# Kernel optimization log

Measured on AMD Instinct MI355X. Metric: run time of the kernel, lower is better.

The kernel has to match this reference:

```python
import jax, jax.numpy as jnp
import numpy as np

B, S, D, H, HD, KVH, FF = 2, 2048, 2048, 16, 128, 1, 8192
EPS = 1e-6
ROPE_BASE = 10000.0
NEG = -1e9


def _rms_norm(x, w):
    return x * jax.lax.rsqrt(jnp.mean(x * x, axis=-1, keepdims=True) + EPS) * w


def _rope(t):
    # t: [B, S, H, HD]; standard rotate-half RoPE
    half = HD // 2
    inv_freq = ROPE_BASE ** (-jnp.arange(0, HD, 2, dtype=jnp.float32) / HD)  # [half]
    ang = jnp.arange(S, dtype=jnp.float32)[:, None] * inv_freq               # [S, half]
    cos = jnp.concatenate([jnp.cos(ang), jnp.cos(ang)], axis=-1)[None, :, None, :]
    sin = jnp.concatenate([jnp.sin(ang), jnp.sin(ang)], axis=-1)[None, :, None, :]
    t1, t2 = t[..., :half], t[..., half:]
    rot = jnp.concatenate([-t2, t1], axis=-1)
    return t * cos + rot * sin


def _alibi_bias():
    # slopes for power-of-two head count: 2^(-8*(h+1)/H)
    slopes = 2.0 ** (-8.0 * (jnp.arange(H, dtype=jnp.float32) + 1.0) / H)    # [H]
    pos = jnp.arange(S, dtype=jnp.float32)
    dist = jnp.abs(pos[:, None] - pos[None, :])                              # [S, S]
    return (-slopes[:, None, None] * dist)[None]                             # [1, H, S, S]


def setup_inputs() -> dict:
    key = jax.random.key(0)
    ks = jax.random.split(key, 8)
    sc = lambda fan: 1.0 / np.sqrt(fan)
    x = jax.random.normal(ks[0], (B, S, D), jnp.float32)
    causal = jnp.where(jnp.tril(jnp.ones((S, S), bool)), 0.0, NEG).astype(jnp.float32)[None, None]
    return {
        "x": x,
        "mask": causal,                                                       # [1,1,S,S]
        "w_norm1": jnp.ones((D,), jnp.float32),
        "w_norm2": jnp.ones((D,), jnp.float32),
        "q_w": jax.random.normal(ks[1], (D, D), jnp.float32) * sc(D),        # [out,in] torch layout
        "kv_w": jax.random.normal(ks[2], (KVH * HD * 2, D), jnp.float32) * sc(D),
        "o_w": jax.random.normal(ks[3], (D, D), jnp.float32) * sc(D),
        "w1": jax.random.normal(ks[4], (FF, D), jnp.float32) * sc(D),
        "w2": jax.random.normal(ks[5], (FF, D), jnp.float32) * sc(D),
        "w3": jax.random.normal(ks[6], (D, FF), jnp.float32) * sc(FF),
    }


def reference(x, mask, w_norm1, w_norm2, q_w, kv_w, o_w, w1, w2, w3):
    # --- attention sub-block (pre-norm) ---
    h = _rms_norm(x, w_norm1)
    q = (h @ q_w.T).reshape(B, S, H, HD)                                      # [B,S,H,HD]
    kv = (h @ kv_w.T).reshape(B, S, KVH, 2, HD)
    k = jnp.broadcast_to(kv[:, :, :, 0, :], (B, S, H, HD))                    # MQA expand
    v = jnp.broadcast_to(kv[:, :, :, 1, :], (B, S, H, HD))
    q, k = _rope(q), _rope(k)
    scores = jnp.einsum('bshd,bthd->bhst', q, k) / np.sqrt(HD)                # [B,H,S,S]
    scores = scores + _alibi_bias() + mask
    attn = jax.nn.softmax(scores, axis=-1)
    out = jnp.einsum('bhst,bthd->bshd', attn, v).reshape(B, S, D)
    x = x + out @ o_w.T
    # --- SwiGLU FFN sub-block (pre-norm) ---
    h2 = _rms_norm(x, w_norm2)
    gated = jax.nn.silu(h2 @ w1.T) * (h2 @ w2.T)                              # [B,S,FF]
    return x + gated @ w3.T
```

## Files before the change

### kernel.cpp

```cpp
#include <hip/hip_runtime.h>
#include <stdint.h>

#define NB 2
#define NS 2048
#define ND 2048
#define NH 16
#define NHD 128
#define NFF 8192
#define NBS (NB*NS)
#define NQKV 2304

typedef unsigned short u16;
typedef __attribute__((ext_vector_type(8))) short bf16x8;
typedef __attribute__((ext_vector_type(4))) unsigned short u16x4;
typedef __attribute__((ext_vector_type(4))) float f32x4;

__device__ __forceinline__ u16 f2bf(float f) {
  union { float f; unsigned u; } v; v.f = f;
  unsigned r = v.u + 0x7fffu + ((v.u >> 16) & 1u);
  return (u16)(r >> 16);
}
__device__ __forceinline__ float bf2f(u16 h) {
  union { unsigned u; float f; } v; v.u = ((unsigned)h) << 16;
  return v.f;
}
__device__ __forceinline__ void async_cp16(const void* g, void* l) {
  __builtin_amdgcn_global_load_lds((const __attribute__((address_space(1))) void*)g,
                                   (__attribute__((address_space(3))) void*)l, 16, 0, 0);
}

__global__ void cvt_bf16_kernel(const float* __restrict__ in, u16* __restrict__ out, int n4) {
  int i = blockIdx.x * blockDim.x + threadIdx.x;
  if (i >= n4) return;
  float4 v = reinterpret_cast<const float4*>(in)[i];
  u16x4 o; o.x = f2bf(v.x); o.y = f2bf(v.y); o.z = f2bf(v.z); o.w = f2bf(v.w);
  reinterpret_cast<u16x4*>(out)[i] = o;
}

__global__ __launch_bounds__(256) void rmsnorm_kernel(const float* __restrict__ x,
                                                      const float* __restrict__ w,
                                                      u16* __restrict__ out) {
  const int row = blockIdx.x, tid = threadIdx.x;
  const float* xr = x + (size_t)row * ND;
  float4 a = *reinterpret_cast<const float4*>(xr + tid * 8);
  float4 b = *reinterpret_cast<const float4*>(xr + tid * 8 + 4);
  float ss = a.x*a.x + a.y*a.y + a.z*a.z + a.w*a.w
           + b.x*b.x + b.y*b.y + b.z*b.z + b.w*b.w;
#pragma unroll
  for (int off = 32; off > 0; off >>= 1) ss += __shfl_down(ss, off);
  __shared__ float red[4];
  __shared__ float rinv_s;
  if ((tid & 63) == 0) red[tid >> 6] = ss;
  __syncthreads();
  if (tid == 0) rinv_s = rsqrtf((red[0] + red[1] + red[2] + red[3]) * (1.0f / ND) + 1e-6f);
  __syncthreads();
  const float rinv = rinv_s;
  const float* wr = w + tid * 8;
  u16* orow = out + (size_t)row * ND + tid * 8;
  float vs[8] = {a.x, a.y, a.z, a.w, b.x, b.y, b.z, b.w};
#pragma unroll
  for (int j = 0; j < 8; ++j) orow[j] = f2bf(vs[j] * rinv * wr[j]);
}

__global__ void rope_table_kernel(float* __restrict__ cosT, float* __restrict__ sinT) {
  int i = blockIdx.x * blockDim.x + threadIdx.x;
  if (i >= NS * 64) return;
  int s = i >> 6, d = i & 63;
  float freq = expf(-(float)d * (9.210340371976184f / 64.0f));
  float ang = (float)s * freq;
  cosT[i] = cosf(ang);
  sinT[i] = sinf(ang);
}

__global__ void rope_q_kernel(const u16* __restrict__ qkvraw, const float* __restrict__ cosT,
                              const float* __restrict__ sinT, u16* __restrict__ qout) {
  int i = blockIdx.x * blockDim.x + threadIdx.x;
  if (i >= NB * NS * NH * 64) return;
  int d = i & 63, h = (i >> 6) & 15, s = (i >> 10) & (NS - 1), b = i >> 21;
  size_t rrow = ((size_t)(b * NS + s)) * NQKV + h * NHD;
  float t1 = bf2f(qkvraw[rrow + d]);
  float t2 = bf2f(qkvraw[rrow + d + 64]);
  float c = cosT[(s << 6) + d], sn = sinT[(s << 6) + d];
  const float scale = 0.08838834764831845f;
  size_t orow = (((size_t)(b * NH + h)) * NS + s) * NHD;
  qout[orow + d]      = f2bf((t1 * c - t2 * sn) * scale);
  qout[orow + d + 64] = f2bf((t2 * c + t1 * sn) * scale);
}

__global__ void rope_kv_kernel(const u16* __restrict__ qkvraw, const float* __restrict__ cosT,
                               const float* __restrict__ sinT, u16* __restrict__ kout,
                               u16* __restrict__ vtout) {
  int i = blockIdx.x * blockDim.x + threadIdx.x;
  if (i >= NB * NS * 64) return;
  int d = i & 63, s = (i >> 6) & (NS - 1), b = i >> 17;
  size_t rrow = ((size_t)(b * NS + s)) * NQKV + ND;
  float t1 = bf2f(qkvraw[rrow + d]);
  float t2 = bf2f(qkvraw[rrow + d + 64]);
  float c = cosT[(s << 6) + d], sn = sinT[(s << 6) + d];
  size_t orow = ((size_t)(b * NS + s)) * NHD;
  kout[orow + d]      = f2bf(t1 * c - t2 * sn);
  kout[orow + d + 64] = f2bf(t2 * c + t1 * sn);
  vtout[((size_t)(b * 128 + d)) * NS + s]      = qkvraw[rrow + 128 + d];
  vtout[((size_t)(b * 128 + d + 64)) * NS + s] = qkvraw[rrow + 128 + d + 64];
}

template <int EPI>
__global__ __launch_bounds__(256) void gemm3_kernel(const u16* __restrict__ A,
                                                    const u16* __restrict__ W,
                                                    void* Out, const void* Aux,
                                                    int M, int N, int K) {
  __shared__ __align__(16) char As[128 * 128];
  __shared__ __align__(16) char Bs[128 * 128];
  const int tid = threadIdx.x, wave = tid >> 6, lane = tid & 63;
  const int lm = lane & 15, lg = lane >> 4;

  int bx, by;
  {
    const int gx = gridDim.x;
    if ((gx & 7) == 0) {
      const int id = blockIdx.y * gx + blockIdx.x;
      const int xcd = id & 7, rank = id >> 3;
      const int cw = gx >> 3;
      bx = xcd * cw + rank % cw;
      by = rank / cw;
    } else { bx = blockIdx.x; by = blockIdx.y; }
  }
  const int m0 = by * 128, n0 = bx * 128;
  const int wr = wave >> 1, wc = wave & 1;

  f32x4 acc[4][4];
#pragma unroll
  for (int i = 0; i < 4; ++i)
#pragma unroll
    for (int j = 0; j < 4; ++j) acc[i][j] = (f32x4){0.f, 0.f, 0.f, 0.f};

  for (int k0 = 0; k0 < K; k0 += 64) {
#pragma unroll
    for (int p = 0; p < 4; ++p) {
      int X = p * 4096 + tid * 16;
      int r = X >> 7;
      int sw = ((X >> 4) ^ (X >> 7)) & 7;
      async_cp16(A + (size_t)(m0 + r) * K + k0 + sw * 8, As + p * 4096 + wave * 1024);
      async_cp16(W + (size_t)(n0 + r) * K + k0 + sw * 8, Bs + p * 4096 + wave * 1024);
    }
    __syncthreads();
#pragma unroll
    for (int ks = 0; ks < 2; ++ks) {
      bf16x8 a[4], b[4];
#pragma unroll
      for (int i = 0; i < 4; ++i) {
        const int ra = wr * 64 + i * 16 + lm;
        const int sa = (ks * 4 + lg) ^ (ra & 7);
        a[i] = *(const bf16x8*)(As + ra * 128 + sa * 16);
        const int rb = wc * 64 + i * 16 + lm;
        const int sb = (ks * 4 + lg) ^ (rb & 7);
        b[i] = *(const bf16x8*)(Bs + rb * 128 + sb * 16);
      }
#pragma unroll
      for (int i = 0; i < 4; ++i)
#pragma unroll
        for (int j = 0; j < 4; ++j)
          acc[i][j] = __builtin_amdgcn_mfma_f32_16x16x32_bf16(a[i], b[j], acc[i][j], 0, 0, 0);
    }
    __syncthreads();
  }

#pragma unroll
  for (int i = 0; i < 4; ++i) {
    const int row_b = m0 + wr * 64 + i * 16 + lg * 4;
#pragma unroll
    for (int j = 0; j < 4; ++j) {
      const int col = n0 + wc * 64 + j * 16 + lm;
#pragma unroll
      for (int r = 0; r < 4; ++r) {
        size_t idx = (size_t)(row_b + r) * N + col;
        float v = acc[i][j][r];
        if constexpr (EPI == 0) {
          ((u16*)Out)[idx] = f2bf(v);
        } else if constexpr (EPI == 1) {
          ((float*)Out)[idx] = v + ((const float*)Aux)[idx];
        } else {
          float a1 = bf2f(((const u16*)Aux)[idx]);
          float s = a1 / (1.0f + expf(-a1));
          ((u16*)Out)[idx] = f2bf(s * v);
        }
      }
    }
  }
}

__global__ __launch_bounds__(256) void attn_kernel(const u16* __restrict__ q,
                                                   const u16* __restrict__ kg,
                                                   const u16* __restrict__ vt,
                                                   u16* __restrict__ out) {
  __shared__ __align__(16) u16 Klds[64 * 128];
  __shared__ __align__(16) u16 Vlds[128 * 64];
  __shared__ __align__(16) u16 Plds[4][16 * 72];
  const int tid = threadIdx.x, wave = tid >> 6, lane = tid & 63;
  const int qt = (gridDim.x - 1) - blockIdx.x;
  const int q0 = qt * 64;
  const int bh = blockIdx.y, b = bh >> 4, h = bh & 15;
  const float slope = exp2f(-0.5f * (float)(h + 1));
  const int lm = lane & 15, lg = lane >> 4;
  const int crow = lg * 4;

  bf16x8 qf[4];
  {
    const int qrow = q0 + wave * 16 + lm;
    const u16* qbase = q + ((size_t)bh * NS + qrow) * NHD + lg * 8;
#pragma unroll
    for (int kc = 0; kc < 4; ++kc) qf[kc] = *(const bf16x8*)(qbase + kc * 32);
  }

  float Mr[4], Lr[4];
  f32x4 O[8];
#pragma unroll
  for (int r = 0; r < 4; ++r) { Mr[r] = -__builtin_inff(); Lr[r] = 0.f; }
#pragma unroll
  for (int t = 0; t < 8; ++t) O[t] = (f32x4){0.f, 0.f, 0.f, 0.f};

  const int kslotK = tid & 15;
  const int kvK    = tid >> 4;
  const int sV     = tid & 7;
  const int dV     = tid >> 3;
  u16* pw = Plds[wave];

  const int ntiles = qt + 1;
  for (int t0 = 0; t0 < ntiles; ++t0) {
    const int kv0 = t0 * 64;
    __syncthreads();
#pragma unroll
    for (int p = 0; p < 4; ++p) {
      int kv = p * 16 + kvK;
      const u16* src = kg + ((size_t)b * NS + kv0 + kv) * NHD + ((kslotK ^ (kv & 7)) * 8);
      async_cp16(src, (char*)Klds + p * 4096 + wave * 1024);
    }
#pragma unroll
    for (int p = 0; p < 4; ++p) {
      int d = p * 32 + dV;
      const u16* src = vt + ((size_t)b * 128 + d) * NS + kv0 + ((sV ^ (d & 7)) * 8);
      async_cp16(src, (char*)Vlds + p * 4096 + wave * 1024);
    }
    __syncthreads();

    f32x4 sc[4];
#pragma unroll
    for (int sub = 0; sub < 4; ++sub) sc[sub] = (f32x4){0.f, 0.f, 0.f, 0.f};
#pragma unroll
    for (int sub = 0; sub < 4; ++sub) {
      const int kv = sub * 16 + lm;
#pragma unroll
      for (int kc = 0; kc < 4; ++kc) {
        const int slot = (kc * 4 + lg) ^ (kv & 7);
        bf16x8 kf = *(const bf16x8*)((const char*)Klds + kv * 256 + slot * 16);
        sc[sub] = __builtin_amdgcn_mfma_f32_16x16x32_bf16(qf[kc], kf, sc[sub], 0, 0, 0);
      }
    }

    float esc[4], pp[4][4];
#pragma unroll
    for (int r = 0; r < 4; ++r) {
      const int sq = q0 + wave * 16 + crow + r;
      float v[4];
#pragma unroll
      for (int sub = 0; sub < 4; ++sub) {
        const int kc_ = kv0 + sub * 16 + lm;
        v[sub] = (kc_ <= sq) ? sc[sub][r] - slope * (float)(sq - kc_) : -1e9f;
      }
      float mx = fmaxf(fmaxf(v[0], v[1]), fmaxf(v[2], v[3]));
      mx = fmaxf(mx, __shfl_xor(mx, 1));
      mx = fmaxf(mx, __shfl_xor(mx, 2));
      mx = fmaxf(mx, __shfl_xor(mx, 4));
      mx = fmaxf(mx, __shfl_xor(mx, 8));
      const float newM = fmaxf(Mr[r], mx);
      esc[r] = __expf(Mr[r] - newM);
      float rs = 0.f;
#pragma unroll
      for (int sub = 0; sub < 4; ++sub) { pp[sub][r] = __expf(v[sub] - newM); rs += pp[sub][r]; }
      rs += __shfl_xor(rs, 1);
      rs += __shfl_xor(rs, 2);
      rs += __shfl_xor(rs, 4);
      rs += __shfl_xor(rs, 8);
      Lr[r] = Lr[r] * esc[r] + rs;
      Mr[r] = newM;
    }
#pragma unroll
    for (int t = 0; t < 8; ++t) {
      O[t][0] *= esc[0]; O[t][1] *= esc[1]; O[t][2] *= esc[2]; O[t][3] *= esc[3];
    }

#pragma unroll
    for (int sub = 0; sub < 4; ++sub)
#pragma unroll
      for (int r = 0; r < 4; ++r)
        pw[(crow + r) * 72 + sub * 16 + lm] = f2bf(pp[sub][r]);

    bf16x8 pa0 = *(const bf16x8*)&pw[lm * 72 + lg * 8];
    bf16x8 pa1 = *(const bf16x8*)&pw[lm * 72 + 32 + lg * 8];
#pragma unroll
    for (int dt = 0; dt < 8; ++dt) {
      const int d = dt * 16 + lm;
      const int s0 = (lg) ^ (d & 7);
      const int s1 = (4 + lg) ^ (d & 7);
      bf16x8 vf0 = *(const bf16x8*)((const char*)Vlds + d * 128 + s0 * 16);
      bf16x8 vf1 = *(const bf16x8*)((const char*)Vlds + d * 128 + s1 * 16);
      O[dt] = __builtin_amdgcn_mfma_f32_16x16x32_bf16(pa0, vf0, O[dt], 0, 0, 0);
      O[dt] = __builtin_amdgcn_mfma_f32_16x16x32_bf16(pa1, vf1, O[dt], 0, 0, 0);
    }
  }

#pragma unroll
  for (int dt = 0; dt < 8; ++dt) {
#pragma unroll
    for (int r = 0; r < 4; ++r) {
      const int sq = q0 + wave * 16 + crow + r;
      out[((size_t)b * NS + sq) * ND + h * NHD + dt * 16 + lm] = f2bf(O[dt][r] / Lr[r]);
    }
  }
}

extern "C" void kernel_launch(void* const* d_in, const int* in_sizes, int n_in,
                              void* d_out, int out_size, void* d_ws, size_t ws_size,
                              hipStream_t stream) {
  const float* x   = (const float*)d_in[0];
  const float* wn1 = (const float*)d_in[2];
  const float* wn2 = (const float*)d_in[3];
  const float* qw  = (const float*)d_in[4];
  const float* kvw = (const float*)d_in[5];
  const float* ow  = (const float*)d_in[6];
  const float* w1  = (const float*)d_in[7];
  const float* w2  = (const float*)d_in[8];
  const float* w3  = (const float*)d_in[9];
  float* out = (float*)d_out;

  const size_t MiB = 1024 * 1024;
  const size_t NEED = 161 * MiB;
  if (ws_size < NEED) return;

  char* ws = (char*)d_ws;
  u16*   R_W    = (u16*)(ws);
  u16*   QKVRAW = (u16*)(ws + 48 * MiB);
  u16*   AO     = QKVRAW;
  u16*   A1     = (u16*)(ws + 48 * MiB);
  u16*   QB     = (u16*)(ws + 112 * MiB);
  u16*   KB     = (u16*)(ws + 128 * MiB);
  u16*   VT     = (u16*)(ws + 129 * MiB);
  float* X2     = (float*)(ws + 112 * MiB);
  u16*   Hbf    = (u16*)(ws + 144 * MiB);
  float* COS    = (float*)(ws + 160 * MiB);
  float* SIN    = (float*)(ws + 160 * MiB + 512 * 1024);

  auto cvt = [&](const float* src, u16* dst, size_t n) {
    int n4 = (int)(n / 4);
    cvt_bf16_kernel<<<(n4 + 255) / 256, 256, 0, stream>>>(src, dst, n4);
  };

  rope_table_kernel<<<(NS * 64 + 255) / 256, 256, 0, stream>>>(COS, SIN);

  rmsnorm_kernel<<<NBS, 256, 0, stream>>>(x, wn1, Hbf);

  cvt(qw, R_W, (size_t)ND * ND);
  cvt(kvw, R_W + (size_t)ND * ND, (size_t)256 * ND);
  gemm3_kernel<0><<<dim3(NQKV / 128, NBS / 128), 256, 0, stream>>>(
      Hbf, R_W, (void*)QKVRAW, nullptr, NBS, NQKV, ND);

  rope_q_kernel<<<(NB * NS * NH * 64) / 256, 256, 0, stream>>>(QKVRAW, COS, SIN, QB);
  rope_kv_kernel<<<(NB * NS * 64) / 256, 256, 0, stream>>>(QKVRAW, COS, SIN, KB, VT);

  attn_kernel<<<dim3(NS / 64, NB * NH), 256, 0, stream>>>(QB, KB, VT, AO);

  cvt(ow, R_W, (size_t)ND * ND);
  gemm3_kernel<1><<<dim3(ND / 128, NBS / 128), 256, 0, stream>>>(
      AO, R_W, (void*)X2, (const void*)x, NBS, ND, ND);

  rmsnorm_kernel<<<NBS, 256, 0, stream>>>(X2, wn2, Hbf);

  cvt(w1, R_W, (size_t)NFF * ND);
  gemm3_kernel<0><<<dim3(NFF / 128, NBS / 128), 256, 0, stream>>>(
      Hbf, R_W, (void*)A1, nullptr, NBS, NFF, ND);
  cvt(w2, R_W, (size_t)NFF * ND);
  gemm3_kernel<2><<<dim3(NFF / 128, NBS / 128), 256, 0, stream>>>(
      Hbf, R_W, (void*)A1, (const void*)A1, NBS, NFF, ND);

  cvt(w3, R_W, (size_t)ND * NFF);
  gemm3_kernel<1><<<dim3(ND / 128, NBS / 128), 256, 0, stream>>>(
      A1, R_W, (void*)out, (const void*)X2, NBS, ND, NFF);
}
```

Before: 916.0 us.

## Use single-wave attention blocks reading K/V directly from global memory

Restructures the attention kernel from 4-wave blocks that stage K and V tiles into shared memory with barriers into 1-wave blocks of 16 query rows that load K and V fragments straight from global memory. This removes the __syncthreads and async LDS copies and gives finer-grained causal load balance across many more blocks. In exchange, K/V reuse across the four query sub-tiles is lost, so each wave issues its own global and cache reads, which raises memory traffic. The V loads are strided by NS across lanes, which may coalesce poorly. The causal tile count now rounds up per 16-row group, so the diagonal 64-wide tile is masked but still computed.

```diff
diff --git a/kernel.cpp b/kernel.cpp
--- a/kernel.cpp
+++ b/kernel.cpp
@@ -189,25 +189,22 @@
   }
 }
 
-__global__ __launch_bounds__(256) void attn_kernel(const u16* __restrict__ q,
-                                                   const u16* __restrict__ kg,
-                                                   const u16* __restrict__ vt,
-                                                   u16* __restrict__ out) {
-  __shared__ __align__(16) u16 Klds[64 * 128];
-  __shared__ __align__(16) u16 Vlds[128 * 64];
-  __shared__ __align__(16) u16 Plds[4][16 * 72];
-  const int tid = threadIdx.x, wave = tid >> 6, lane = tid & 63;
-  const int qt = (gridDim.x - 1) - blockIdx.x;
-  const int q0 = qt * 64;
+__global__ __launch_bounds__(64, 4) void attn_kernel(const u16* __restrict__ q,
+                                                     const u16* __restrict__ kg,
+                                                     const u16* __restrict__ vt,
+                                                     u16* __restrict__ out) {
+  __shared__ __align__(16) u16 Plds[16 * 72];
+  const int lane = threadIdx.x & 63;
+  const int q16 = (gridDim.x - 1) - blockIdx.x;
   const int bh = blockIdx.y, b = bh >> 4, h = bh & 15;
   const float slope = exp2f(-0.5f * (float)(h + 1));
   const int lm = lane & 15, lg = lane >> 4;
   const int crow = lg * 4;
+  const int qrow0 = q16 * 16;
 
   bf16x8 qf[4];
   {
-    const int qrow = q0 + wave * 16 + lm;
-    const u16* qbase = q + ((size_t)bh * NS + qrow) * NHD + lg * 8;
+    const u16* qbase = q + ((size_t)bh * NS + qrow0 + lm) * NHD + lg * 8;
 #pragma unroll
     for (int kc = 0; kc < 4; ++kc) qf[kc] = *(const bf16x8*)(qbase + kc * 32);
   }
@@ -219,40 +216,22 @@
 #pragma unroll
   for (int t = 0; t < 8; ++t) O[t] = (f32x4){0.f, 0.f, 0.f, 0.f};
 
-  const int kslotK = tid & 15;
-  const int kvK    = tid >> 4;
-  const int sV     = tid & 7;
-  const int dV     = tid >> 3;
-  u16* pw = Plds[wave];
-
-  const int ntiles = qt + 1;
+  const u16* kbase = kg + (size_t)b * NS * NHD;
+  const u16* vbase = vt + (size_t)b * 128 * NS;
+
+  const int ntiles = q16 / 4 + 1;
   for (int t0 = 0; t0 < ntiles; ++t0) {
     const int kv0 = t0 * 64;
-    __syncthreads();
-#pragma unroll
-    for (int p = 0; p < 4; ++p) {
-      int kv = p * 16 + kvK;
-      const u16* src = kg + ((size_t)b * NS + kv0 + kv) * NHD + ((kslotK ^ (kv & 7)) * 8);
-      async_cp16(src, (char*)Klds + p * 4096 + wave * 1024);
-    }
-#pragma unroll
-    for (int p = 0; p < 4; ++p) {
-      int d = p * 32 + dV;
-      const u16* src = vt + ((size_t)b * 128 + d) * NS + kv0 + ((sV ^ (d & 7)) * 8);
-      async_cp16(src, (char*)Vlds + p * 4096 + wave * 1024);
-    }
-    __syncthreads();
 
     f32x4 sc[4];
 #pragma unroll
     for (int sub = 0; sub < 4; ++sub) sc[sub] = (f32x4){0.f, 0.f, 0.f, 0.f};
 #pragma unroll
     for (int sub = 0; sub < 4; ++sub) {
-      const int kv = sub * 16 + lm;
+      const u16* kr = kbase + (size_t)(kv0 + sub * 16 + lm) * NHD + lg * 8;
 #pragma unroll
       for (int kc = 0; kc < 4; ++kc) {
-        const int slot = (kc * 4 + lg) ^ (kv & 7);
-        bf16x8 kf = *(const bf16x8*)((const char*)Klds + kv * 256 + slot * 16);
+        bf16x8 kf = *(const bf16x8*)(kr + kc * 32);
         sc[sub] = __builtin_amdgcn_mfma_f32_16x16x32_bf16(qf[kc], kf, sc[sub], 0, 0, 0);
       }
     }
@@ -260,7 +239,7 @@
     float esc[4], pp[4][4];
 #pragma unroll
     for (int r = 0; r < 4; ++r) {
-      const int sq = q0 + wave * 16 + crow + r;
+      const int sq = qrow0 + crow + r;
       float v[4];
 #pragma unroll
       for (int sub = 0; sub < 4; ++sub) {
@@ -293,17 +272,16 @@
     for (int sub = 0; sub < 4; ++sub)
 #pragma unroll
       for (int r = 0; r < 4; ++r)
-        pw[(crow + r) * 72 + sub * 16 + lm] = f2bf(pp[sub][r]);
-
-    bf16x8 pa0 = *(const bf16x8*)&pw[lm * 72 + lg * 8];
-    bf16x8 pa1 = *(const bf16x8*)&pw[lm * 72 + 32 + lg * 8];
+        Plds[(crow + r) * 72 + sub * 16 + lm] = f2bf(pp[sub][r]);
+
+    bf16x8 pa0 = *(const bf16x8*)&Plds[lm * 72 + lg * 8];
+    bf16x8 pa1 = *(const bf16x8*)&Plds[lm * 72 + 32 + lg * 8];
+
 #pragma unroll
     for (int dt = 0; dt < 8; ++dt) {
-      const int d = dt * 16 + lm;
-      const int s0 = (lg) ^ (d & 7);
-      const int s1 = (4 + lg) ^ (d & 7);
-      bf16x8 vf0 = *(const bf16x8*)((const char*)Vlds + d * 128 + s0 * 16);
-      bf16x8 vf1 = *(const bf16x8*)((const char*)Vlds + d * 128 + s1 * 16);
+      const u16* vr = vbase + (size_t)(dt * 16 + lm) * NS + kv0 + lg * 8;
+      bf16x8 vf0 = *(const bf16x8*)(vr);
+      bf16x8 vf1 = *(const bf16x8*)(vr + 32);
       O[dt] = __builtin_amdgcn_mfma_f32_16x16x32_bf16(pa0, vf0, O[dt], 0, 0, 0);
       O[dt] = __builtin_amdgcn_mfma_f32_16x16x32_bf16(pa1, vf1, O[dt], 0, 0, 0);
     }
@@ -313,7 +291,7 @@
   for (int dt = 0; dt < 8; ++dt) {
 #pragma unroll
     for (int r = 0; r < 4; ++r) {
-      const int sq = q0 + wave * 16 + crow + r;
+      const int sq = qrow0 + crow + r;
       out[((size_t)b * NS + sq) * ND + h * NHD + dt * 16 + lm] = f2bf(O[dt][r] / Lr[r]);
     }
   }
@@ -367,7 +345,7 @@
   rope_q_kernel<<<(NB * NS * NH * 64) / 256, 256, 0, stream>>>(QKVRAW, COS, SIN, QB);
   rope_kv_kernel<<<(NB * NS * 64) / 256, 256, 0, stream>>>(QKVRAW, COS, SIN, KB, VT);
 
-  attn_kernel<<<dim3(NS / 64, NB * NH), 256, 0, stream>>>(QB, KB, VT, AO);
+  attn_kernel<<<dim3(NS / 16, NB * NH), 64, 0, stream>>>(QB, KB, VT, AO);
 
   cvt(ow, R_W, (size_t)ND * ND);
   gemm3_kernel<1><<<dim3(ND / 128, NBS / 128), 256, 0, stream>>>(
```

After: 1.174 ms. 1.28x slower.
